# Kernel optimization log

Hardware: AMD Instinct MI355X
Metric: run time of the kernel (lower is better)

The kernel has to match this reference:

```python
import jax, jax.numpy as jnp
import numpy as np

B, T, C, NH, HS, NL, VOCAB = 4, 1024, 768, 12, 64, 6, 128
PRIMES = [2, 3, 5, 7, 11, 13, 17, 19, 23, 29]
NEG_INF = jnp.finfo(jnp.float32).min


def _build_lut(t):
    # lut[n, i] = v_{p_i}(n), p-adic valuation of position n
    lut = np.zeros((t + 1, len(PRIMES)), np.float32)
    for pi, p in enumerate(PRIMES):
        nn = np.arange(t + 1, dtype=np.int64)
        nn[0] = 1  # v_p(0) treated as 0
        while (nn % p == 0).any():
            d = nn % p == 0
            lut[d, pi] += 1.0
            nn[d] //= p
    return lut


def _build_buffers(t):
    lut = _build_lut(t)
    vl = lut[1 : t + 1]  # positions 1..T, [T, 10]
    res = np.minimum(vl[:, None, :], vl[None, :, :]).sum(-1)  # [T, T]
    causal = np.tril(np.ones((t, t), dtype=bool))
    allowed = ((res > 0) | np.eye(t, dtype=bool)) & causal
    rbias = (np.log1p(res) * allowed).astype(np.float32)
    return vl.astype(np.float32), rbias, allowed


def setup_inputs() -> dict:
    key = jax.random.key(0)
    ks = jax.random.split(key, 16)
    s = 0.02
    vl, rbias, allowed = _build_buffers(T)
    return {
        "idx": jax.random.randint(ks[0], (B, T), 0, VOCAB, dtype=jnp.int32),
        "tok_emb": jax.random.normal(ks[1], (VOCAB, C)) * s,
        "pe_w": jax.random.normal(ks[2], (10, C)) * s,
        "pe_b": jnp.zeros((C,)),
        "vlut": jnp.asarray(vl),
        "rbias": jnp.asarray(rbias),
        "allowed": jnp.asarray(allowed),
        "ln1_g": jnp.ones((NL, C)),
        "ln1_b": jnp.zeros((NL, C)),
        "qw": jax.random.normal(ks[3], (NL, NH, C, HS)) * s,
        "kw": jax.random.normal(ks[4], (NL, NH, C, HS)) * s,
        "vw": jax.random.normal(ks[5], (NL, NH, C, HS)) * s,
        "proj_w": jax.random.normal(ks[6], (NL, C, C)) * s,
        "proj_b": jnp.zeros((NL, C)),
        "ln2_g": jnp.ones((NL, C)),
        "ln2_b": jnp.zeros((NL, C)),
        "ff1_w": jax.random.normal(ks[7], (NL, C, 4 * C)) * s,
        "ff1_b": jnp.zeros((NL, 4 * C)),
        "ff2_w": jax.random.normal(ks[8], (NL, 4 * C, C)) * s,
        "ff2_b": jnp.zeros((NL, C)),
        "lnf_g": jnp.ones((C,)),
        "lnf_b": jnp.zeros((C,)),
        "head_w": jax.random.normal(ks[9], (C, VOCAB)) * s,
        "head_b": jnp.zeros((VOCAB,)),
    }


def _ln(x, g, b, eps=1e-5):
    m = x.mean(-1, keepdims=True)
    v = ((x - m) ** 2).mean(-1, keepdims=True)
    return (x - m) * jax.lax.rsqrt(v + eps) * g + b


def reference(idx, tok_emb, pe_w, pe_b, vlut, rbias, allowed,
              ln1_g, ln1_b, qw, kw, vw, proj_w, proj_b,
              ln2_g, ln2_b, ff1_w, ff1_b, ff2_w, ff2_b,
              lnf_g, lnf_b, head_w, head_b):
    # token embedding + spectral positional encoding
    x = tok_emb[idx] + (vlut @ pe_w + pe_b)  # [B, T, C]
    scale = C ** (-0.5)  # NOTE: source scales by full embed dim, not head_size
    for l in range(NL):
        h = _ln(x, ln1_g[l], ln1_b[l])
        q = jnp.einsum("btc,hcd->bhtd", h, qw[l])
        k = jnp.einsum("btc,hcd->bhtd", h, kw[l])
        v = jnp.einsum("btc,hcd->bhtd", h, vw[l])
        w = jnp.einsum("bhtd,bhsd->bhts", q, k) * scale + rbias  # [B,H,T,T]
        w = jnp.where(allowed, w, NEG_INF)
        a = jax.nn.softmax(w, axis=-1)
        o = jnp.einsum("bhts,bhsd->bhtd", a, v)
        o = o.transpose(0, 2, 1, 3).reshape(x.shape[0], x.shape[1], C)
        x = x + o @ proj_w[l] + proj_b[l]
        h2 = _ln(x, ln2_g[l], ln2_b[l])
        x = x + jax.nn.gelu(h2 @ ff1_w[l] + ff1_b[l], approximate=False) @ ff2_w[l] + ff2_b[l]
    return _ln(x, lnf_g, lnf_b) @ head_w + head_b  # [B, T, VOCAB]
```

## Files before the change

### kernel.cpp

```cpp
#include <hip/hip_runtime.h>
#include <hip/hip_bf16.h>
#include <math.h>


#define Bz 4
#define Tz 1024
#define Cz 768
#define NHz 12
#define HSz 64
#define NLz 6
#define VOCABz 128
#define NTOK (Bz * Tz)

typedef __hip_bfloat16 bf16;
typedef __attribute__((ext_vector_type(8))) __bf16 bf16x8;
typedef __attribute__((ext_vector_type(4))) float f32x4;

#define MFMA16(a, b, c) __builtin_amdgcn_mfma_f32_16x16x32_bf16(a, b, c, 0, 0, 0)

__device__ __forceinline__ float bf2f(bf16 x) { return __bfloat162float(x); }
__device__ __forceinline__ bf16 f2bf(float x) { return __float2bfloat16(x); }
__device__ __forceinline__ float ldx(const void* p, size_t i, int f) {
  return f ? bf2f(((const bf16*)p)[i]) : ((const float*)p)[i];
}
__device__ __forceinline__ void async16(const bf16* g, bf16* l) {
  __builtin_amdgcn_global_load_lds(
      (const __attribute__((address_space(1))) unsigned int*)g,
      (__attribute__((address_space(3))) unsigned int*)l, 16, 0, 0);
}

__global__ void detect_kernel(const void* g1, int* flag) {
  if (threadIdx.x == 0) {
    const unsigned short* p = (const unsigned short*)g1;
    int cnt = 0;
    for (int i = 0; i < 64; i++) cnt += (p[i] == 0x3F80u) ? 1 : 0;
    *flag = (cnt >= 60) ? 1 : 0;
  }
}

#define NCONV 15
struct CPack {
  const void* s[NCONV];
  bf16* d[NCONV];
  int n[NCONV];
};
__global__ __launch_bounds__(256) void convert_all(CPack p, const int* __restrict__ flagp) {
  int f = *flagp;
  int stride = gridDim.x * 256;
#pragma unroll 1
  for (int t = 0; t < NCONV; t++) {
    int n = p.n[t];
    const void* src = p.s[t];
    bf16* dst = p.d[t];
    for (int i = blockIdx.x * 256 + threadIdx.x; i < n; i += stride)
      dst[i] = f ? ((const bf16*)src)[i] : f2bf(((const float*)src)[i]);
  }
}

__global__ __launch_bounds__(256) void transpose_tiled(
    const void* __restrict__ src, bf16* __restrict__ dst, int R, int C,
    size_t s_mat, size_t d_base, size_t d_l, size_t d_h, int hmod,
    const int* __restrict__ flagp) {
  __shared__ bf16 t[64][65];
  int f = *flagp;
  int c0 = blockIdx.x * 64, r0 = blockIdx.y * 64;
  int z = blockIdx.z;
  size_t so = (size_t)z * s_mat;
  size_t dofs = d_base + (size_t)(z / hmod) * d_l + (size_t)(z % hmod) * d_h;
  int tr = threadIdx.x >> 2;
  int tc = (threadIdx.x & 3) * 16;
  size_t sbase = so + (size_t)(r0 + tr) * C + c0 + tc;
#pragma unroll
  for (int u = 0; u < 16; u++) t[tr][tc + u] = f2bf(ldx(src, sbase + u, f));
  __syncthreads();
  int wc = threadIdx.x >> 2;
  int wr = (threadIdx.x & 3) * 16;
  bf16* dp = dst + dofs + (size_t)(c0 + wc) * R + r0 + wr;
#pragma unroll
  for (int u = 0; u < 16; u++) dp[u] = t[wr + u][wc];
}

__global__ __launch_bounds__(256) void embed_kernel(
    const int* __restrict__ idx, const bf16* __restrict__ tok_emb,
    const bf16* __restrict__ pe_w, const bf16* __restrict__ pe_b,
    const bf16* __restrict__ vlut, float* __restrict__ x_res) {
  int row = blockIdx.x;
  int t = row % Tz;
  int tok = idx[row];
  float vl[10];
#pragma unroll
  for (int p = 0; p < 10; p++) vl[p] = bf2f(vlut[t * 10 + p]);
  for (int c = threadIdx.x; c < Cz; c += 256) {
    float acc = bf2f(tok_emb[(size_t)tok * Cz + c]) + bf2f(pe_b[c]);
#pragma unroll
    for (int p = 0; p < 10; p++) acc += vl[p] * bf2f(pe_w[p * Cz + c]);
    x_res[(size_t)row * Cz + c] = acc;
  }
}

__global__ __launch_bounds__(256) void ln_kernel(
    const float* __restrict__ x, const bf16* __restrict__ g,
    const bf16* __restrict__ b, bf16* __restrict__ out) {
  int w = threadIdx.x >> 6, lane = threadIdx.x & 63;
  int row = blockIdx.x * 4 + w;
  const float* xr = x + (size_t)row * Cz;
  float v[12];
  float s1 = 0.0f, s2 = 0.0f;
#pragma unroll
  for (int i = 0; i < 12; i++) {
    v[i] = xr[lane + i * 64];
    s1 += v[i];
    s2 += v[i] * v[i];
  }
#pragma unroll
  for (int off = 32; off >= 1; off >>= 1) {
    s1 += __shfl_xor(s1, off);
    s2 += __shfl_xor(s2, off);
  }
  float m = s1 * (1.0f / Cz);
  float var = s2 * (1.0f / Cz) - m * m;
  float inv = rsqrtf(var + 1e-5f);
  bf16* orow = out + (size_t)row * Cz;
#pragma unroll
  for (int i = 0; i < 12; i++) {
    int c = lane + i * 64;
    orow[c] = f2bf((v[i] - m) * inv * bf2f(g[c]) + bf2f(b[c]));
  }
}

template <int MT>
__global__ __launch_bounds__(256) void gemm_mfma(
    const bf16* __restrict__ A, const bf16* __restrict__ Wt,
    const bf16* __restrict__ bias, float* __restrict__ resid,
    void* __restrict__ out, int M, int N, int K, int mode,
    const int* __restrict__ flagp) {
  constexpr int TM = MT * 32;
  constexpr int API = MT / 2;
  __shared__ bf16 ldsA[2][TM * 32];
  __shared__ bf16 ldsB[2][4096];
  int tid = threadIdx.x;
  int lane = tid & 63, w = tid >> 6;
  int wm = (w >> 1) * (MT * 16), wn = (w & 1) * 64;
  int q = lane >> 4, ln = lane & 15;
  int m0 = blockIdx.y * TM, n0 = blockIdx.x * 128;

  const bf16* gA[API];
  const bf16* gB[2];
#pragma unroll
  for (int p = 0; p < API; p++) {
    int o = w * (API * 1024) + p * 1024 + lane * 16;
    int rp = o >> 7, pp = (o >> 4) & 7;
    int pl = pp ^ (rp & 7);
    int row = rp * 2 + (pl >> 2);
    int cb = pl & 3;
    gA[p] = A + (size_t)(m0 + row) * K + cb * 8;
  }
#pragma unroll
  for (int p = 0; p < 2; p++) {
    int o = w * 2048 + p * 1024 + lane * 16;
    int rp = o >> 7, pp = (o >> 4) & 7;
    int pl = pp ^ (rp & 7);
    int row = rp * 2 + (pl >> 2);
    int cb = pl & 3;
    gB[p] = Wt + (size_t)(n0 + row) * K + cb * 8;
  }
  int ppf = (((ln & 1) << 2) | q) ^ (ln >> 1);
  int aoff = wm * 32 + (ln >> 1) * 64 + ppf * 8;
  int boff = wn * 32 + (ln >> 1) * 64 + ppf * 8;

  f32x4 acc[MT][4] = {};
#pragma unroll
  for (int p = 0; p < API; p++)
    async16(gA[p], &ldsA[0][w * (API * 512) + p * 512]);
#pragma unroll
  for (int p = 0; p < 2; p++)
    async16(gB[p], &ldsB[0][w * 1024 + p * 512]);
  int cur = 0;
  for (int k0 = 0; k0 < K; k0 += 32) {
    __syncthreads();
    if (k0 + 32 < K) {
      int nxt = cur ^ 1;
#pragma unroll
      for (int p = 0; p < API; p++)
        async16(gA[p] + k0 + 32, &ldsA[nxt][w * (API * 512) + p * 512]);
#pragma unroll
      for (int p = 0; p < 2; p++)
        async16(gB[p] + k0 + 32, &ldsB[nxt][w * 1024 + p * 512]);
    }
    bf16x8 af[MT], bfr[4];
#pragma unroll
    for (int i = 0; i < MT; i++)
      af[i] = *(const bf16x8*)&ldsA[cur][aoff + i * 512];
#pragma unroll
    for (int j = 0; j < 4; j++)
      bfr[j] = *(const bf16x8*)&ldsB[cur][boff + j * 512];
#pragma unroll
    for (int i = 0; i < MT; i++)
#pragma unroll
      for (int j = 0; j < 4; j++)
        acc[i][j] = MFMA16(af[i], bfr[j], acc[i][j]);
    cur ^= 1;
  }
  int f = *flagp;
  float bj[4];
#pragma unroll
  for (int j = 0; j < 4; j++)
    bj[j] = bias ? bf2f(bias[n0 + wn + j * 16 + ln]) : 0.0f;
#pragma unroll
  for (int i = 0; i < MT; i++) {
#pragma unroll
    for (int j = 0; j < 4; j++) {
      int col = n0 + wn + j * 16 + ln;
#pragma unroll
      for (int r = 0; r < 4; r++) {
        int row = m0 + wm + i * 16 + q * 4 + r;
        float v = acc[i][j][r] + bj[j];
        size_t oi = (size_t)row * N + col;
        if (mode == 0) {
          ((bf16*)out)[oi] = f2bf(v);
        } else if (mode == 1) {
          ((bf16*)out)[oi] = f2bf(v * 0.5f * (1.0f + erff(v * 0.70710678118f)));
        } else if (mode == 2) {
          resid[oi] += v;
        } else {
          if (f) ((bf16*)out)[oi] = f2bf(v);
          else ((float*)out)[oi] = v;
        }
      }
    }
  }
}

#define ATS 72
__global__ __launch_bounds__(256) void transpose_v(
    const bf16* __restrict__ qkv, bf16* __restrict__ Vt) {
  __shared__ bf16 tile[64][ATS];
  int tid = threadIdx.x;
  int s0 = blockIdx.x * 64, bh = blockIdx.y;
  int b = bh / NHz, h = bh % NHz;
  int row = tid >> 2, c0 = (tid & 3) * 16;
  const bf16* src = qkv + ((size_t)(b * Tz + s0 + row)) * (3 * Cz) + 2 * Cz + h * HSz + c0;
  *(uint4*)&tile[row][c0] = *(const uint4*)src;
  *(uint4*)&tile[row][c0 + 8] = *(const uint4*)(src + 8);
  __syncthreads();
  int d = tid >> 2, sc0 = (tid & 3) * 16;
  unsigned int u[8];
#pragma unroll
  for (int m = 0; m < 8; m++) {
    unsigned int lo = *(const unsigned short*)&tile[sc0 + 2 * m][d];
    unsigned int hi = *(const unsigned short*)&tile[sc0 + 2 * m + 1][d];
    u[m] = lo | (hi << 16);
  }
  bf16* dst = Vt + ((size_t)bh * HSz + d) * Tz + s0 + sc0;
  ((uint4*)dst)[0] = make_uint4(u[0], u[1], u[2], u[3]);
  ((uint4*)dst)[1] = make_uint4(u[4], u[5], u[6], u[7]);
}

__global__ __launch_bounds__(256) void attn_flash(
    const bf16* __restrict__ qkv, const bf16* __restrict__ Vt,
    const bf16* __restrict__ rbias, bf16* __restrict__ attn_out) {
  __shared__ bf16 Qs[64][ATS];
  __shared__ bf16 Ks[64][ATS];
  __shared__ bf16 Vs[64][ATS];
  __shared__ bf16 Ps[4][16][ATS];
  int tid = threadIdx.x;
  int lane = tid & 63, w = tid >> 6;
  int q = lane >> 4, ln = lane & 15;
  int qt = (int)gridDim.x - 1 - (int)blockIdx.x;
  int t0 = qt * 64, bh = blockIdx.y;
  int b = bh / NHz, h = bh % NHz;
  const float scale = 0.03608439182435161f;
  int srow = tid >> 2, sc = (tid & 3) * 16;
  {
    const bf16* src = qkv + ((size_t)(b * Tz + t0 + srow)) * (3 * Cz) + h * HSz + sc;
    *(uint4*)&Qs[srow][sc] = *(const uint4*)src;
    *(uint4*)&Qs[srow][sc + 8] = *(const uint4*)(src + 8);
  }
  float mrow[4], lrow[4];
  f32x4 Oacc[4] = {};
#pragma unroll
  for (int r = 0; r < 4; r++) { mrow[r] = -3.0e38f; lrow[r] = 0.0f; }
  int t_base = t0 + w * 16 + q * 4;
  int nk = qt + 1;

  const bf16* kcol = qkv + (size_t)b * Tz * (3 * Cz) + Cz + h * HSz + sc;
  const bf16* vrow = Vt + ((size_t)bh * HSz + srow) * Tz + sc;
  uint4 ka, kb, va, vb2;
  {
    const bf16* kp = kcol + (size_t)srow * (3 * Cz);
    ka = *(const uint4*)kp;
    kb = *(const uint4*)(kp + 8);
    va = *(const uint4*)vrow;
    vb2 = *(const uint4*)(vrow + 8);
  }
  for (int kt = 0; kt < nk; kt++) {
    __syncthreads();
    *(uint4*)&Ks[srow][sc] = ka;
    *(uint4*)&Ks[srow][sc + 8] = kb;
    *(uint4*)&Vs[srow][sc] = va;
    *(uint4*)&Vs[srow][sc + 8] = vb2;
    __syncthreads();
    if (kt + 1 < nk) {
      const bf16* kp = kcol + (size_t)(((kt + 1) * 64) + srow) * (3 * Cz);
      ka = *(const uint4*)kp;
      kb = *(const uint4*)(kp + 8);
      const bf16* vp = vrow + (kt + 1) * 64;
      va = *(const uint4*)vp;
      vb2 = *(const uint4*)(vp + 8);
    }
    int s0 = kt * 64;
    f32x4 sacc[4] = {};
#pragma unroll
    for (int ks = 0; ks < 64; ks += 32) {
      bf16x8 aq = *(const bf16x8*)&Qs[w * 16 + ln][ks + q * 8];
#pragma unroll
      for (int j = 0; j < 4; j++) {
        bf16x8 bk = *(const bf16x8*)&Ks[j * 16 + ln][ks + q * 8];
        sacc[j] = MFMA16(aq, bk, sacc[j]);
      }
    }
    float sval[4][4];
#pragma unroll
    for (int j = 0; j < 4; j++) {
      int s_col = s0 + j * 16 + ln;
#pragma unroll
      for (int r = 0; r < 4; r++) {
        int t_row = t_base + r;
        float rb = bf2f(rbias[(size_t)t_row * Tz + s_col]);
        float v = sacc[j][r] * scale + rb;
        bool ok = (s_col <= t_row) && ((rb > 0.0f) || (s_col == t_row));
        sval[j][r] = ok ? v : -3.0e38f;
      }
    }
    float rmax[4];
#pragma unroll
    for (int r = 0; r < 4; r++)
      rmax[r] = fmaxf(fmaxf(sval[0][r], sval[1][r]), fmaxf(sval[2][r], sval[3][r]));
#pragma unroll
    for (int msk = 8; msk >= 1; msk >>= 1)
#pragma unroll
      for (int r = 0; r < 4; r++)
        rmax[r] = fmaxf(rmax[r], __shfl_xor(rmax[r], msk));
    float nme[4], alpha[4];
#pragma unroll
    for (int r = 0; r < 4; r++) {
      float nm = fmaxf(mrow[r], rmax[r]);
      nme[r] = (nm < -1.0e37f) ? 0.0f : nm;
      alpha[r] = (mrow[r] < -1.0e37f) ? 0.0f : __expf(mrow[r] - nm);
      mrow[r] = nm;
    }
    float pf[4][4];
    float psum[4] = {0.f, 0.f, 0.f, 0.f};
#pragma unroll
    for (int j = 0; j < 4; j++)
#pragma unroll
      for (int r = 0; r < 4; r++) {
        float p = __expf(sval[j][r] - nme[r]);
        pf[j][r] = p;
        psum[r] += p;
      }
#pragma unroll
    for (int msk = 8; msk >= 1; msk >>= 1)
#pragma unroll
      for (int r = 0; r < 4; r++) psum[r] += __shfl_xor(psum[r], msk);
#pragma unroll
    for (int r = 0; r < 4; r++) lrow[r] = alpha[r] * lrow[r] + psum[r];
#pragma unroll
    for (int jd = 0; jd < 4; jd++)
#pragma unroll
      for (int r = 0; r < 4; r++) Oacc[jd][r] *= alpha[r];
#pragma unroll
    for (int j = 0; j < 4; j++)
#pragma unroll
      for (int r = 0; r < 4; r++)
        Ps[w][q * 4 + r][j * 16 + ln] = f2bf(pf[j][r]);
#pragma unroll
    for (int ks = 0; ks < 64; ks += 32) {
      bf16x8 pa = *(const bf16x8*)&Ps[w][ln][ks + q * 8];
#pragma unroll
      for (int jd = 0; jd < 4; jd++) {
        bf16x8 vb = *(const bf16x8*)&Vs[jd * 16 + ln][ks + q * 8];
        Oacc[jd] = MFMA16(pa, vb, Oacc[jd]);
      }
    }
  }
#pragma unroll
  for (int r = 0; r < 4; r++) {
    float inv = 1.0f / lrow[r];
    int t_row = t_base + r;
#pragma unroll
    for (int jd = 0; jd < 4; jd++) {
      attn_out[(size_t)(b * Tz + t_row) * Cz + h * HSz + jd * 16 + ln] =
          f2bf(Oacc[jd][r] * inv);
    }
  }
}

extern "C" void kernel_launch(void* const* d_in, const int* in_sizes, int n_in,
                              void* d_out, int out_size, void* d_ws, size_t ws_size,
                              hipStream_t stream) {
  const int* idx = (const int*)d_in[0];
  int p0 = 7;
  if (n_in == 23) p0 = 6;
  else if (in_sizes[6] != Tz * Tz) p0 = 6;

  const void* r_tok_emb = d_in[1];
  const void* r_pe_w = d_in[2];
  const void* r_pe_b = d_in[3];
  const void* r_vlut = d_in[4];
  const void* r_rbias = d_in[5];
  const void* r_ln1_g = d_in[p0 + 0];
  const void* r_ln1_b = d_in[p0 + 1];
  const void* r_qw = d_in[p0 + 2];
  const void* r_kw = d_in[p0 + 3];
  const void* r_vw = d_in[p0 + 4];
  const void* r_proj_w = d_in[p0 + 5];
  const void* r_proj_b = d_in[p0 + 6];
  const void* r_ln2_g = d_in[p0 + 7];
  const void* r_ln2_b = d_in[p0 + 8];
  const void* r_ff1_w = d_in[p0 + 9];
  const void* r_ff1_b = d_in[p0 + 10];
  const void* r_ff2_w = d_in[p0 + 11];
  const void* r_ff2_b = d_in[p0 + 12];
  const void* r_lnf_g = d_in[p0 + 13];
  const void* r_lnf_b = d_in[p0 + 14];
  const void* r_head_w = d_in[p0 + 15];
  const void* r_head_b = d_in[p0 + 16];

  char* wsp = (char*)d_ws;
  auto alloc = [&](size_t bytes) {
    char* p = wsp;
    wsp += (bytes + 255) & ~(size_t)255;
    return (void*)p;
  };
  int* flag = (int*)alloc(256);
  float* x_res = (float*)alloc((size_t)NTOK * Cz * 4);
  bf16* h = (bf16*)alloc((size_t)NTOK * Cz * 2);
  bf16* qkv = (bf16*)alloc((size_t)NTOK * 3 * Cz * 2);
  bf16* attn = (bf16*)alloc((size_t)NTOK * Cz * 2);
  bf16* ffm = (bf16*)alloc((size_t)NTOK * 4 * Cz * 2);
  bf16* Vt = (bf16*)alloc((size_t)Bz * NHz * HSz * Tz * 2);
  bf16* wqkv_t = (bf16*)alloc((size_t)NLz * 3 * Cz * Cz * 2);
  bf16* proj_t = (bf16*)alloc((size_t)NLz * Cz * Cz * 2);
  bf16* ff1_t = (bf16*)alloc((size_t)NLz * 4 * Cz * Cz * 2);
  bf16* ff2_t = (bf16*)alloc((size_t)NLz * 4 * Cz * Cz * 2);
  bf16* head_t = (bf16*)alloc((size_t)VOCABz * Cz * 2);
  bf16* tok_emb = (bf16*)alloc((size_t)VOCABz * Cz * 2);
  bf16* pe_w = (bf16*)alloc(10 * Cz * 2);
  bf16* pe_b = (bf16*)alloc(Cz * 2);
  bf16* vlut = (bf16*)alloc(Tz * 10 * 2);
  bf16* rbias = (bf16*)alloc((size_t)Tz * Tz * 2);
  bf16* ln1_g = (bf16*)alloc(NLz * Cz * 2);
  bf16* ln1_b = (bf16*)alloc(NLz * Cz * 2);
  bf16* proj_b = (bf16*)alloc(NLz * Cz * 2);
  bf16* ln2_g = (bf16*)alloc(NLz * Cz * 2);
  bf16* ln2_b = (bf16*)alloc(NLz * Cz * 2);
  bf16* ff1_b = (bf16*)alloc(NLz * 4 * Cz * 2);
  bf16* ff2_b = (bf16*)alloc(NLz * Cz * 2);
  bf16* lnf_g = (bf16*)alloc(Cz * 2);
  bf16* lnf_b = (bf16*)alloc(Cz * 2);
  bf16* head_b = (bf16*)alloc(VOCABz * 2);

  detect_kernel<<<1, 64, 0, stream>>>(r_ln1_g, flag);

  CPack cp;
  const void* csrc[NCONV] = {r_tok_emb, r_pe_w, r_pe_b, r_vlut, r_rbias,
                             r_ln1_g, r_ln1_b, r_proj_b, r_ln2_g, r_ln2_b,
                             r_ff1_b, r_ff2_b, r_lnf_g, r_lnf_b, r_head_b};
  bf16* cdst[NCONV] = {tok_emb, pe_w, pe_b, vlut, rbias,
                       ln1_g, ln1_b, proj_b, ln2_g, ln2_b,
                       ff1_b, ff2_b, lnf_g, lnf_b, head_b};
  int cn[NCONV] = {VOCABz * Cz, 10 * Cz, Cz, Tz * 10, Tz * Tz,
                   NLz * Cz, NLz * Cz, NLz * Cz, NLz * Cz, NLz * Cz,
                   NLz * 4 * Cz, NLz * Cz, Cz, Cz, VOCABz};
  for (int i = 0; i < NCONV; i++) { cp.s[i] = csrc[i]; cp.d[i] = cdst[i]; cp.n[i] = cn[i]; }
  convert_all<<<1024, 256, 0, stream>>>(cp, flag);

  for (int g = 0; g < 3; g++) {
    const void* src = (g == 0) ? r_qw : (g == 1) ? r_kw : r_vw;
    transpose_tiled<<<dim3(1, Cz / 64, NLz * NHz), 256, 0, stream>>>(
        src, wqkv_t, Cz, HSz, (size_t)Cz * HSz,
        (size_t)g * Cz * Cz, (size_t)3 * Cz * Cz, (size_t)HSz * Cz, NHz, flag);
  }
  transpose_tiled<<<dim3(Cz / 64, Cz / 64, NLz), 256, 0, stream>>>(
      r_proj_w, proj_t, Cz, Cz, (size_t)Cz * Cz, 0, (size_t)Cz * Cz, 0, 1, flag);
  transpose_tiled<<<dim3(4 * Cz / 64, Cz / 64, NLz), 256, 0, stream>>>(
      r_ff1_w, ff1_t, Cz, 4 * Cz, (size_t)4 * Cz * Cz, 0, (size_t)4 * Cz * Cz, 0, 1, flag);
  transpose_tiled<<<dim3(Cz / 64, 4 * Cz / 64, NLz), 256, 0, stream>>>(
      r_ff2_w, ff2_t, 4 * Cz, Cz, (size_t)4 * Cz * Cz, 0, (size_t)4 * Cz * Cz, 0, 1, flag);
  transpose_tiled<<<dim3(VOCABz / 64, Cz / 64, 1), 256, 0, stream>>>(
      r_head_w, head_t, Cz, VOCABz, 0, 0, 0, 0, 1, flag);

  embed_kernel<<<NTOK, 256, 0, stream>>>(idx, tok_emb, pe_w, pe_b, vlut, x_res);

  for (int l = 0; l < NLz; l++) {
    ln_kernel<<<NTOK / 4, 256, 0, stream>>>(x_res, ln1_g + l * Cz, ln1_b + l * Cz, h);
    gemm_mfma<4><<<dim3(3 * Cz / 128, NTOK / 128), 256, 0, stream>>>(
        h, wqkv_t + (size_t)l * 3 * Cz * Cz, nullptr, nullptr, qkv,
        NTOK, 3 * Cz, Cz, 0, flag);
    transpose_v<<<dim3(Tz / 64, Bz * NHz), 256, 0, stream>>>(qkv, Vt);
    attn_flash<<<dim3(Tz / 64, Bz * NHz), 256, 0, stream>>>(qkv, Vt, rbias, attn);
    gemm_mfma<2><<<dim3(Cz / 128, NTOK / 64), 256, 0, stream>>>(
        attn, proj_t + (size_t)l * Cz * Cz, proj_b + l * Cz, x_res, nullptr,
        NTOK, Cz, Cz, 2, flag);
    ln_kernel<<<NTOK / 4, 256, 0, stream>>>(x_res, ln2_g + l * Cz, ln2_b + l * Cz, h);
    gemm_mfma<4><<<dim3(4 * Cz / 128, NTOK / 128), 256, 0, stream>>>(
        h, ff1_t + (size_t)l * 4 * Cz * Cz, ff1_b + (size_t)l * 4 * Cz, nullptr,
        ffm, NTOK, 4 * Cz, Cz, 1, flag);
    gemm_mfma<2><<<dim3(Cz / 128, NTOK / 64), 256, 0, stream>>>(
        ffm, ff2_t + (size_t)l * 4 * Cz * Cz, ff2_b + l * Cz, x_res, nullptr,
        NTOK, Cz, 4 * Cz, 2, flag);
  }
  ln_kernel<<<NTOK / 4, 256, 0, stream>>>(x_res, lnf_g, lnf_b, h);
  gemm_mfma<2><<<dim3(VOCABz / 128, NTOK / 64), 256, 0, stream>>>(
      h, head_t, head_b, nullptr, d_out, NTOK, VOCABz, Cz, 3, flag);
}
```

Measured before the change: 1.815 ms.

## Precompute masked bias table and fuse V transpose into QKV GEMM epilogue

Builds a combined bias-plus-mask table once per call, with disallowed positions set to a large negative value. The attention kernel stages each 64x64 bias tile into shared memory through coalesced prefetch alongside K and V, replacing the scattered per-element global bias loads and mask arithmetic. The QKV GEMM gains an epilogue mode that writes V directly in transposed layout, which removes the separate transpose_v kernel and its round trip through memory. The transposed V stores are uncoalesced scalar writes, and the extra shared tile raises LDS use, which may lower occupancy.

```diff
diff --git a/kernel.cpp b/kernel.cpp
--- a/kernel.cpp
+++ b/kernel.cpp
@@ -57,6 +57,16 @@
   }
 }
 
+__global__ __launch_bounds__(256) void build_bm(
+    const bf16* __restrict__ rbias, bf16* __restrict__ bm) {
+  int i = blockIdx.x * 256 + threadIdx.x;
+  int t = i >> 10, s = i & 1023;
+  bf16 rb16 = rbias[i];
+  float rb = bf2f(rb16);
+  bool ok = (s <= t) && ((rb > 0.0f) || (s == t));
+  bm[i] = ok ? rb16 : f2bf(-3.0e38f);
+}
+
 __global__ __launch_bounds__(256) void transpose_tiled(
     const void* __restrict__ src, bf16* __restrict__ dst, int R, int C,
     size_t s_mat, size_t d_base, size_t d_l, size_t d_h, int hmod,
@@ -222,6 +232,15 @@
           ((bf16*)out)[oi] = f2bf(v * 0.5f * (1.0f + erff(v * 0.70710678118f)));
         } else if (mode == 2) {
           resid[oi] += v;
+        } else if (mode == 5) {
+          if (col < 2 * Cz) {
+            ((bf16*)out)[oi] = f2bf(v);
+          } else {
+            int nn = col - 2 * Cz;
+            int hh = nn >> 6, dd = nn & 63;
+            int bb = row >> 10, tt = row & 1023;
+            ((bf16*)resid)[(((size_t)(bb * NHz + hh)) * HSz + dd) * Tz + tt] = f2bf(v);
+          }
         } else {
           if (f) ((bf16*)out)[oi] = f2bf(v);
           else ((float*)out)[oi] = v;
@@ -232,36 +251,13 @@
 }
 
 #define ATS 72
-__global__ __launch_bounds__(256) void transpose_v(
-    const bf16* __restrict__ qkv, bf16* __restrict__ Vt) {
-  __shared__ bf16 tile[64][ATS];
-  int tid = threadIdx.x;
-  int s0 = blockIdx.x * 64, bh = blockIdx.y;
-  int b = bh / NHz, h = bh % NHz;
-  int row = tid >> 2, c0 = (tid & 3) * 16;
-  const bf16* src = qkv + ((size_t)(b * Tz + s0 + row)) * (3 * Cz) + 2 * Cz + h * HSz + c0;
-  *(uint4*)&tile[row][c0] = *(const uint4*)src;
-  *(uint4*)&tile[row][c0 + 8] = *(const uint4*)(src + 8);
-  __syncthreads();
-  int d = tid >> 2, sc0 = (tid & 3) * 16;
-  unsigned int u[8];
-#pragma unroll
-  for (int m = 0; m < 8; m++) {
-    unsigned int lo = *(const unsigned short*)&tile[sc0 + 2 * m][d];
-    unsigned int hi = *(const unsigned short*)&tile[sc0 + 2 * m + 1][d];
-    u[m] = lo | (hi << 16);
-  }
-  bf16* dst = Vt + ((size_t)bh * HSz + d) * Tz + s0 + sc0;
-  ((uint4*)dst)[0] = make_uint4(u[0], u[1], u[2], u[3]);
-  ((uint4*)dst)[1] = make_uint4(u[4], u[5], u[6], u[7]);
-}
-
 __global__ __launch_bounds__(256) void attn_flash(
     const bf16* __restrict__ qkv, const bf16* __restrict__ Vt,
-    const bf16* __restrict__ rbias, bf16* __restrict__ attn_out) {
+    const bf16* __restrict__ bm, bf16* __restrict__ attn_out) {
   __shared__ bf16 Qs[64][ATS];
   __shared__ bf16 Ks[64][ATS];
   __shared__ bf16 Vs[64][ATS];
+  __shared__ bf16 Bs[64][ATS];
   __shared__ bf16 Ps[4][16][ATS];
   int tid = threadIdx.x;
   int lane = tid & 63, w = tid >> 6;
@@ -285,13 +281,16 @@
 
   const bf16* kcol = qkv + (size_t)b * Tz * (3 * Cz) + Cz + h * HSz + sc;
   const bf16* vrow = Vt + ((size_t)bh * HSz + srow) * Tz + sc;
-  uint4 ka, kb, va, vb2;
+  const bf16* brow = bm + (size_t)(t0 + srow) * Tz + sc;
+  uint4 ka, kb, va, vb2, ba, bb2;
   {
     const bf16* kp = kcol + (size_t)srow * (3 * Cz);
     ka = *(const uint4*)kp;
     kb = *(const uint4*)(kp + 8);
     va = *(const uint4*)vrow;
     vb2 = *(const uint4*)(vrow + 8);
+    ba = *(const uint4*)brow;
+    bb2 = *(const uint4*)(brow + 8);
   }
   for (int kt = 0; kt < nk; kt++) {
     __syncthreads();
@@ -299,16 +298,21 @@
     *(uint4*)&Ks[srow][sc + 8] = kb;
     *(uint4*)&Vs[srow][sc] = va;
     *(uint4*)&Vs[srow][sc + 8] = vb2;
+    *(uint4*)&Bs[srow][sc] = ba;
+    *(uint4*)&Bs[srow][sc + 8] = bb2;
     __syncthreads();
     if (kt + 1 < nk) {
-      const bf16* kp = kcol + (size_t)(((kt + 1) * 64) + srow) * (3 * Cz);
+      int s1 = (kt + 1) * 64;
+      const bf16* kp = kcol + (size_t)(s1 + srow) * (3 * Cz);
       ka = *(const uint4*)kp;
       kb = *(const uint4*)(kp + 8);
-      const bf16* vp = vrow + (kt + 1) * 64;
+      const bf16* vp = vrow + s1;
       va = *(const uint4*)vp;
       vb2 = *(const uint4*)(vp + 8);
-    }
-    int s0 = kt * 64;
+      const bf16* bp = brow + s1;
+      ba = *(const uint4*)bp;
+      bb2 = *(const uint4*)(bp + 8);
+    }
     f32x4 sacc[4] = {};
 #pragma unroll
     for (int ks = 0; ks < 64; ks += 32) {
@@ -321,17 +325,10 @@
     }
     float sval[4][4];
 #pragma unroll
-    for (int j = 0; j < 4; j++) {
-      int s_col = s0 + j * 16 + ln;
-#pragma unroll
-      for (int r = 0; r < 4; r++) {
-        int t_row = t_base + r;
-        float rb = bf2f(rbias[(size_t)t_row * Tz + s_col]);
-        float v = sacc[j][r] * scale + rb;
-        bool ok = (s_col <= t_row) && ((rb > 0.0f) || (s_col == t_row));
-        sval[j][r] = ok ? v : -3.0e38f;
-      }
-    }
+    for (int j = 0; j < 4; j++)
+#pragma unroll
+      for (int r = 0; r < 4; r++)
+        sval[j][r] = fmaf(sacc[j][r], scale, bf2f(Bs[w * 16 + q * 4 + r][j * 16 + ln]));
     float rmax[4];
 #pragma unroll
     for (int r = 0; r < 4; r++)
@@ -346,7 +343,7 @@
     for (int r = 0; r < 4; r++) {
       float nm = fmaxf(mrow[r], rmax[r]);
       nme[r] = (nm < -1.0e37f) ? 0.0f : nm;
-      alpha[r] = (mrow[r] < -1.0e37f) ? 0.0f : __expf(mrow[r] - nm);
+      alpha[r] = __expf(mrow[r] - nm);
       mrow[r] = nm;
     }
     float pf[4][4];
@@ -450,6 +447,7 @@
   bf16* pe_b = (bf16*)alloc(Cz * 2);
   bf16* vlut = (bf16*)alloc(Tz * 10 * 2);
   bf16* rbias = (bf16*)alloc((size_t)Tz * Tz * 2);
+  bf16* bmx = (bf16*)alloc((size_t)Tz * Tz * 2);
   bf16* ln1_g = (bf16*)alloc(NLz * Cz * 2);
   bf16* ln1_b = (bf16*)alloc(NLz * Cz * 2);
   bf16* proj_b = (bf16*)alloc(NLz * Cz * 2);
@@ -475,6 +473,7 @@
                    NLz * 4 * Cz, NLz * Cz, Cz, Cz, VOCABz};
   for (int i = 0; i < NCONV; i++) { cp.s[i] = csrc[i]; cp.d[i] = cdst[i]; cp.n[i] = cn[i]; }
   convert_all<<<1024, 256, 0, stream>>>(cp, flag);
+  build_bm<<<Tz * Tz / 256, 256, 0, stream>>>(rbias, bmx);
 
   for (int g = 0; g < 3; g++) {
     const void* src = (g == 0) ? r_qw : (g == 1) ? r_kw : r_vw;
@@ -496,10 +495,9 @@
   for (int l = 0; l < NLz; l++) {
     ln_kernel<<<NTOK / 4, 256, 0, stream>>>(x_res, ln1_g + l * Cz, ln1_b + l * Cz, h);
     gemm_mfma<4><<<dim3(3 * Cz / 128, NTOK / 128), 256, 0, stream>>>(
-        h, wqkv_t + (size_t)l * 3 * Cz * Cz, nullptr, nullptr, qkv,
-        NTOK, 3 * Cz, Cz, 0, flag);
-    transpose_v<<<dim3(Tz / 64, Bz * NHz), 256, 0, stream>>>(qkv, Vt);
-    attn_flash<<<dim3(Tz / 64, Bz * NHz), 256, 0, stream>>>(qkv, Vt, rbias, attn);
+        h, wqkv_t + (size_t)l * 3 * Cz * Cz, nullptr, (float*)Vt, qkv,
+        NTOK, 3 * Cz, Cz, 5, flag);
+    attn_flash<<<dim3(Tz / 64, Bz * NHz), 256, 0, stream>>>(qkv, Vt, bmx, attn);
     gemm_mfma<2><<<dim3(Cz / 128, NTOK / 64), 256, 0, stream>>>(
         attn, proj_t + (size_t)l * Cz * Cz, proj_b + l * Cz, x_res, nullptr,
         NTOK, Cz, Cz, 2, flag);
```

After: 1.806 ms. No clear change (-0.5%).
